# Kernel optimization log

Measured on AMD Instinct MI355X. Metric: run time of the kernel, lower is better.

The kernel has to match this reference:

```python
import jax, jax.numpy as jnp
import numpy as np

B, T, D, H = 2, 2048, 1024, 16
DH = D // H  # 64


def setup_inputs() -> dict:
    key = jax.random.key(0)
    ks = jax.random.split(key, 11)
    s = 1.0 / np.sqrt(D)
    return {
        "q": jax.random.normal(ks[0], (B, T, D), jnp.float32),
        "k": jax.random.normal(ks[1], (B, T, D), jnp.float32),
        "v": jax.random.normal(ks[2], (B, T, D), jnp.float32),
        "Wq": jax.random.normal(ks[3], (D, D), jnp.float32) * s,
        "bq": jnp.zeros((D,), jnp.float32),
        "Wk": jax.random.normal(ks[4], (D, D), jnp.float32) * s,
        "bk": jnp.zeros((D,), jnp.float32),
        "Wv": jax.random.normal(ks[5], (D, D), jnp.float32) * s,
        "bv": jnp.zeros((D,), jnp.float32),
        "Wo": jax.random.normal(ks[6], (D, D), jnp.float32) * s,
        "bo": jnp.zeros((D,), jnp.float32),
    }


def reference(q, k, v, Wq, bq, Wk, bk, Wv, bv, Wo, bo):
    Bq, Tq, _ = q.shape
    Tk = k.shape[1]
    # projections, split heads: [B, H, T, DH]
    qh = (q @ Wq + bq).reshape(Bq, Tq, H, DH).transpose(0, 2, 1, 3)
    kh = (k @ Wk + bk).reshape(Bq, Tk, H, DH).transpose(0, 2, 1, 3)
    vh = (v @ Wv + bv).reshape(Bq, Tk, H, DH).transpose(0, 2, 1, 3)
    # scores [B, H, Tq, Tk]
    scores = jnp.einsum("bhqd,bhkd->bhqk", qh, kh) / np.sqrt(DH)
    # causal mask with diagonal offset Tk - Tq (matches torch.tril semantics)
    ii = jnp.arange(Tq)[:, None]
    jj = jnp.arange(Tk)[None, :]
    causal = jj <= ii + (Tk - Tq)
    scores = jnp.where(causal, scores, -jnp.inf)
    attn = jax.nn.softmax(scores, axis=-1)
    x = jnp.einsum("bhqk,bhkd->bhqd", attn, vh)  # [B, H, Tq, DH]
    x = x.transpose(0, 2, 1, 3).reshape(Bq, Tq, H * DH)
    return x @ Wo + bo
```

## Files before the change

### kernel.cpp

```cpp
#include <hip/hip_runtime.h>

typedef unsigned short u16;
typedef unsigned int   u32;
typedef __attribute__((ext_vector_type(8)))  short short8;
typedef __attribute__((ext_vector_type(4)))  float f32x4;
typedef __attribute__((ext_vector_type(16))) float f32x16;
typedef __attribute__((ext_vector_type(2)))  u32 uint2v;
typedef __attribute__((ext_vector_type(4)))  u32 uint4v;

#define DEV __device__ __forceinline__

DEV u16 f2bf(float f) {
    u32 u = __builtin_bit_cast(u32, f);
    return (u16)((u + 0x7fffu + ((u >> 16) & 1u)) >> 16);
}
DEV float bf2f(u32 u) { return __builtin_bit_cast(float, u << 16); }
DEV u32 cvtpk(float a, float b) {
    u32 r;
    asm("v_cvt_pk_bf16_f32 %0, %1, %2" : "=v"(r) : "v"(a), "v"(b));
    return r;
}
typedef const __attribute__((address_space(1))) u32 g_u32;
typedef __attribute__((address_space(3))) u32 l_u32;
DEV void gload16(const u16* g, u16* l) {
    __builtin_amdgcn_global_load_lds((g_u32*)g, (l_u32*)l, 16, 0, 0);
}


template<int OMODE>
DEV void gemm_body(const u16* __restrict__ A_, const u16* __restrict__ Bt,
                   const float* __restrict__ bias, float oscale, void* C_) {
    constexpr int Kd = 1024;
    const int m0 = blockIdx.y * 128, n0 = blockIdx.x * 128;
    const int t = threadIdx.x, lane = t & 63, w = t >> 6;
    const int wm = w >> 1, wn = w & 1;
    const int l15 = lane & 15, l4 = lane >> 4;
    __shared__ __align__(16) u16 As[128 * 32];
    __shared__ __align__(16) u16 Bs[128 * 32];
    f32x4 acc[4][4] = {};

    for (int k0 = 0; k0 < Kd; k0 += 32) {
        #pragma unroll
        for (int rnd = 0; rnd < 2; rnd++) {
            int cc = rnd * 256 + t, row = cc >> 2, slot = cc & 3;
            gload16(Bt + (size_t)(n0 + row) * Kd + k0 + slot * 8, Bs + cc * 8);
            gload16(A_ + (size_t)(m0 + row) * Kd + k0 + slot * 8, As + cc * 8);
        }
        __syncthreads();
        short8 af[4], bfr[4];
        #pragma unroll
        for (int i = 0; i < 4; i++) {
            af[i]  = *(const short8*)(As + (wm * 64 + i * 16 + l15) * 32 + l4 * 8);
            bfr[i] = *(const short8*)(Bs + (wn * 64 + i * 16 + l15) * 32 + l4 * 8);
        }
        #pragma unroll
        for (int i = 0; i < 4; i++)
            #pragma unroll
            for (int j = 0; j < 4; j++)
                acc[i][j] = __builtin_amdgcn_mfma_f32_16x16x32_bf16(af[i], bfr[j], acc[i][j], 0, 0, 0);
        __syncthreads();
    }

    #pragma unroll
    for (int i = 0; i < 4; i++) {
        #pragma unroll
        for (int j = 0; j < 4; j++) {
            int col = n0 + wn * 64 + j * 16 + l15;
            int mb  = m0 + wm * 64 + i * 16 + l4 * 4;
            float bv = bias[col];
            if (OMODE == 2) {
                float* C = (float*)C_;
                #pragma unroll
                for (int r = 0; r < 4; r++)
                    C[(size_t)(mb + r) * 1024 + col] = acc[i][j][r] + bv;
            } else if (OMODE == 0) {
                u16* C = (u16*)C_;
                #pragma unroll
                for (int r = 0; r < 4; r++)
                    C[(size_t)(mb + r) * 1024 + col] = f2bf((acc[i][j][r] + bv) * oscale);
            } else if (OMODE == 3) {
                u16* C = (u16*)C_;
                int hh = col >> 6, dd = col & 63;
                int bb = mb >> 11, tt = mb & 2047;
                size_t tile = ((size_t)(bb * 16 + hh) * 64 + (tt >> 5)) * 2048;
                int c = dd >> 4, hi2 = (dd >> 3) & 1, e = dd & 7;
                int lob = tt & 31;
                #pragma unroll
                for (int r = 0; r < 4; r++)
                    C[tile + (size_t)((c * 2 + hi2) * 32 + lob + r) * 8 + e] =
                        f2bf(acc[i][j][r] + bv);
            } else {
                u16* C = (u16*)C_;
                int hh = col >> 6, dd = col & 63;
                int bb = mb >> 11, tt = mb & 2047;
                size_t tile = ((size_t)(bb * 16 + hh) * 64 + (tt >> 5)) * 2048;
                int tin = tt & 31, kc = tin >> 4, hi2 = (tin >> 3) & 1, e0 = tin & 7;
                int c2 = dd >> 5, lo2 = dd & 31;
                size_t off = tile + (size_t)((kc * 2 + c2) * 64 + hi2 * 32 + lo2) * 8 + e0;
                uint2v pp;
                pp[0] = cvtpk(acc[i][j][0] + bv, acc[i][j][1] + bv);
                pp[1] = cvtpk(acc[i][j][2] + bv, acc[i][j][3] + bv);
                *(uint2v*)(C + off) = pp;
            }
        }
    }
}

__global__ __launch_bounds__(256) void k_transw(const float* Wq, const float* Wk,
                                                const float* Wv, const float* Wo, u16* Wt) {
    int z = blockIdx.z;
    const float* W = z == 0 ? Wq : z == 1 ? Wk : z == 2 ? Wv : Wo;
    u16* O = Wt + (size_t)z * 1048576;
    __shared__ float tile[32][33];
    int n0 = blockIdx.x * 32, k0 = blockIdx.y * 32;
    int tx = threadIdx.x, ty = threadIdx.y;
    #pragma unroll
    for (int i = 0; i < 32; i += 8) tile[ty + i][tx] = W[(size_t)(k0 + ty + i) * 1024 + n0 + tx];
    __syncthreads();
    #pragma unroll
    for (int i = 0; i < 32; i += 8) O[(size_t)(n0 + ty + i) * 1024 + k0 + tx] = f2bf(tile[tx][ty + i]);
}

__global__ __launch_bounds__(256) void k_cvt(const float* q, const float* k, const float* v,
                                             u16* Abf) {
    int z = blockIdx.z;
    const float* src = z == 0 ? q : z == 1 ? k : v;
    u16* dst = Abf + (size_t)z * 4194304;
    size_t i = ((size_t)blockIdx.x * 256 + threadIdx.x) * 8;
    float4 a = *(const float4*)(src + i);
    float4 b = *(const float4*)(src + i + 4);
    uint4v o;
    o[0] = cvtpk(a.x, a.y); o[1] = cvtpk(a.z, a.w);
    o[2] = cvtpk(b.x, b.y); o[3] = cvtpk(b.z, b.w);
    *(uint4v*)(dst + i) = o;
}

__global__ __launch_bounds__(256) void k_proj(const u16* Abf, const u16* Wt,
                                              const float* bq, const float* bk,
                                              const float* bv, u16* QKV) {
    int z = blockIdx.z;
    if (z == 2)
        gemm_body<1>(Abf + (size_t)2 * 4194304, Wt + (size_t)2 * 1048576, bv, 1.f,
                     QKV + (size_t)2 * 4194304);
    else if (z == 1)
        gemm_body<3>(Abf + (size_t)4194304, Wt + (size_t)1048576, bk, 1.f,
                     QKV + (size_t)4194304);
    else
        gemm_body<0>(Abf, Wt, bq, 0.125f * 1.44269504088896f, QKV);
}

__global__ __launch_bounds__(256) void k_combine(const u16* Xp, const float* Lp, u16* Xc) {
    size_t idx = (size_t)blockIdx.x * 256 + threadIdx.x;
    size_t e = idx * 8;
    int row = (int)(e >> 10), hh = ((int)e & 1023) >> 6;
    float l0 = Lp[(size_t)row * 16 + hh];
    float l1 = Lp[65536 + (size_t)row * 16 + hh];
    float l2 = Lp[131072 + (size_t)row * 16 + hh];
    float s = 1.0f / (l0 + l1 + l2);
    float w0 = l0 * s, w1 = l1 * s, w2 = l2 * s;
    uint4v x0 = *(const uint4v*)(Xp + e);
    uint4v x1 = *(const uint4v*)(Xp + (size_t)4194304 + e);
    uint4v x2 = *(const uint4v*)(Xp + (size_t)2 * 4194304 + e);
    uint4v o;
    #pragma unroll
    for (int j = 0; j < 4; j++) {
        float a0 = bf2f(x0[j] & 0xffffu) * w0 + bf2f(x1[j] & 0xffffu) * w1
                 + bf2f(x2[j] & 0xffffu) * w2;
        float a1 = bf2f(x0[j] >> 16) * w0 + bf2f(x1[j] >> 16) * w1
                 + bf2f(x2[j] >> 16) * w2;
        o[j] = cvtpk(a0, a1);
    }
    *(uint4v*)(Xc + e) = o;
}

__global__ __launch_bounds__(256) void k_gemm_out(const u16* Xc, const u16* Wt,
                                                  const float* bo, float* out) {
    gemm_body<2>(Xc, Wt, bo, 1.f, out);
}

__global__ __launch_bounds__(256, 3) void k_attn(const u16* __restrict__ Qp,
                                                 const u16* __restrict__ Kp2,
                                                 const u16* __restrict__ Vp2,
                                                 u16* __restrict__ Xp, float* __restrict__ Lp) {
    const int id = (int)blockIdx.x;
    const int bh = id & 31;
    const int j = (id >> 5) & 15;
    const int par = id >> 9;
    const int b = bh >> 4, h = bh & 15;
    const int t = threadIdx.x, lane = t & 63, w = t >> 6;
    const int lo = lane & 31, hi = lane >> 5;
    const int qt = w * 16 + j;
    const int q0 = qt * 32;
    const int NTw = qt + 1;
    const u16* Qb = Qp + (size_t)(b * 2048) * 1024 + h * 64;
    const u16* Kb = Kp2 + (size_t)bh * 64 * 2048;
    const u16* Vb = Vp2 + (size_t)bh * 64 * 2048;

    short8 qf[4];
    #pragma unroll
    for (int c = 0; c < 4; c++)
        qf[c] = *(const short8*)(Qb + (size_t)(q0 + lo) * 1024 + c * 16 + hi * 8);

    f32x16 O0 = {}, O1 = {};
    float lsum = 0.f;
    const int qg = q0 + lo;

#define LOADKV(KF, VF, kt) do {                                                          \
        const u16* kt_ = Kb + (size_t)(kt) * 2048;                                       \
        const u16* vt_ = Vb + (size_t)(kt) * 2048;                                       \
        _Pragma("unroll")                                                                \
        for (int c = 0; c < 4; c++)                                                      \
            KF[c] = *(const short8*)(kt_ + c * 512 + lane * 8);                          \
        _Pragma("unroll")                                                                \
        for (int jj = 0; jj < 4; jj++)                                                   \
            VF[jj] = *(const short8*)(vt_ + jj * 512 + lane * 8);                        \
    } while (0)

#define COMPUTE(KF, VF, kt) do {                                                          \
        f32x16 S = {};                                                                    \
        _Pragma("unroll")                                                                 \
        for (int c = 0; c < 4; c++)                                                       \
            S = __builtin_amdgcn_mfma_f32_32x32x16_bf16(KF[c], qf[c], S, 0, 0, 0);        \
        const bool diag = ((kt) == NTw - 1);                                              \
        _Pragma("unroll")                                                                 \
        for (int kc = 0; kc < 2; kc++) {                                                  \
            float pv[8];                                                                  \
            _Pragma("unroll")                                                             \
            for (int jj = 0; jj < 8; jj++) {                                              \
                int r = kc * 8 + jj;                                                      \
                float s = S[r];                                                           \
                if (diag) {                                                               \
                    int kg = (kt) * 32 + (r & 3) + 8 * (r >> 2) + 4 * hi;                 \
                    s = (kg <= qg) ? s : -1e30f;                                          \
                }                                                                         \
                pv[jj] = __builtin_amdgcn_exp2f(s);                                       \
            }                                                                             \
            lsum += (((pv[0] + pv[1]) + (pv[2] + pv[3])) +                                \
                     ((pv[4] + pv[5]) + (pv[6] + pv[7])));                                \
            u32 w0 = cvtpk(pv[0], pv[1]), w1 = cvtpk(pv[2], pv[3]);                       \
            u32 w2 = cvtpk(pv[4], pv[5]), w3 = cvtpk(pv[6], pv[7]);                       \
            auto r0 = __builtin_amdgcn_permlane32_swap(w0, w2, false, false);             \
            auto r1 = __builtin_amdgcn_permlane32_swap(w1, w3, false, false);             \
            uint4v fw; fw[0] = r0[0]; fw[1] = r1[0]; fw[2] = r0[1]; fw[3] = r1[1];        \
            short8 pf = __builtin_bit_cast(short8, fw);                                   \
            O0 = __builtin_amdgcn_mfma_f32_32x32x16_bf16(pf, VF[kc * 2 + 0], O0, 0, 0, 0);\
            O1 = __builtin_amdgcn_mfma_f32_32x32x16_bf16(pf, VF[kc * 2 + 1], O1, 0, 0, 0);\
        }                                                                                 \
    } while (0)

    {
        short8 kf0[4], vf0[4], kf1[4], vf1[4];
        int kt = par;
        if (kt < NTw) {
            LOADKV(kf0, vf0, kt);
            while (true) {
                if (kt + 3 < NTw) LOADKV(kf1, vf1, kt + 3);
                COMPUTE(kf0, vf0, kt);
                kt += 3;
                if (kt >= NTw) break;
                if (kt + 3 < NTw) LOADKV(kf0, vf0, kt + 3);
                COMPUTE(kf1, vf1, kt);
                kt += 3;
                if (kt >= NTw) break;
            }
        }
    }
#undef LOADKV
#undef COMPUTE

    float ltot = lsum + __shfl_xor(lsum, 32, 64);
    u16* Xb = Xp + (size_t)par * 4194304;
    #pragma unroll
    for (int r = 0; r < 16; r++) {
        int qr = (r & 3) + 8 * (r >> 2) + 4 * hi;
        float lt = __shfl(ltot, qr, 64);
        float linv = lt > 0.f ? 1.f / lt : 0.f;
        size_t rowb = (size_t)(b * 2048 + q0 + qr) * 1024 + h * 64;
        Xb[rowb + lo]      = f2bf(O0[r] * linv);
        Xb[rowb + 32 + lo] = f2bf(O1[r] * linv);
    }
    if (hi == 0)
        Lp[(size_t)par * 65536 + (size_t)(b * 2048 + q0 + lo) * 16 + h] = ltot;
}

extern "C" void kernel_launch(void* const* d_in, const int* in_sizes, int n_in,
                              void* d_out, int out_size, void* d_ws, size_t ws_size,
                              hipStream_t stream) {
    (void)in_sizes; (void)n_in; (void)out_size; (void)ws_size;
    const float* q  = (const float*)d_in[0];
    const float* k  = (const float*)d_in[1];
    const float* v  = (const float*)d_in[2];
    const float* Wq = (const float*)d_in[3];
    const float* bq = (const float*)d_in[4];
    const float* Wk = (const float*)d_in[5];
    const float* bk = (const float*)d_in[6];
    const float* Wv = (const float*)d_in[7];
    const float* bv = (const float*)d_in[8];
    const float* Wo = (const float*)d_in[9];
    const float* bo = (const float*)d_in[10];

    u16*   Wt  = (u16*)d_ws;
    u16*   QKV = Wt + (size_t)4 * 1048576;
    u16*   Abf = QKV + (size_t)3 * 4194304;
    u16*   Xp  = Abf;
    u16*   Xc  = QKV;
    float* Lp  = (float*)(Abf + (size_t)3 * 4194304);

    k_transw<<<dim3(32, 32, 4), dim3(32, 8), 0, stream>>>(Wq, Wk, Wv, Wo, Wt);
    k_cvt<<<dim3(2048, 1, 3), 256, 0, stream>>>(q, k, v, Abf);
    k_proj<<<dim3(8, 32, 3), 256, 0, stream>>>(Abf, Wt, bq, bk, bv, QKV);
    k_attn<<<dim3(1536), 256, 0, stream>>>(QKV, QKV + (size_t)4194304,
                                           QKV + (size_t)2 * 4194304, Xp, Lp);
    k_combine<<<2048, 256, 0, stream>>>(Xp, Lp, Xc);
    k_gemm_out<<<dim3(8, 32), 256, 0, stream>>>(Xc, Wt + (size_t)3 * 1048576,
                                                bo, (float*)d_out);
}
```

Baseline: 126.7 us.

## Pre-pack GEMM operands into MFMA fragment order for contiguous loads

The producer kernels (weight transpose, input convert, combine) now write bf16 operands in a tiled 16x32 fragment-packed layout, so each GEMM k-step loads one contiguous 1KB chunk per 16-row tile. LDS reads become lane-linear and avoid the strided row pattern with its possible bank conflicts. The GEMM template is also turned into a runtime omode branch, which may add branching and register pressure in the epilogue. Producer stores are now scattered, which can reduce their write coalescing.

Result: slower. 135.1 us (+6.6%).

```diff
diff --git a/kernel.cpp b/kernel.cpp
--- a/kernel.cpp
+++ b/kernel.cpp
@@ -27,10 +27,9 @@
 }
 
 
-template<int OMODE>
-DEV void gemm_body(const u16* __restrict__ A_, const u16* __restrict__ Bt,
-                   const float* __restrict__ bias, float oscale, void* C_) {
-    constexpr int Kd = 1024;
+DEV void gemm_body(const u16* __restrict__ Apk, const u16* __restrict__ Bpk,
+                   const float* __restrict__ bias, float oscale, void* C_,
+                   int omode) {
     const int m0 = blockIdx.y * 128, n0 = blockIdx.x * 128;
     const int t = threadIdx.x, lane = t & 63, w = t >> 6;
     const int wm = w >> 1, wn = w & 1;
@@ -39,19 +38,21 @@
     __shared__ __align__(16) u16 Bs[128 * 32];
     f32x4 acc[4][4] = {};
 
-    for (int k0 = 0; k0 < Kd; k0 += 32) {
+    const int rtA = m0 >> 4, rtB = n0 >> 4;
+    for (int k0 = 0; k0 < 1024; k0 += 32) {
+        const int ct = k0 >> 5;
         #pragma unroll
         for (int rnd = 0; rnd < 2; rnd++) {
-            int cc = rnd * 256 + t, row = cc >> 2, slot = cc & 3;
-            gload16(Bt + (size_t)(n0 + row) * Kd + k0 + slot * 8, Bs + cc * 8);
-            gload16(A_ + (size_t)(m0 + row) * Kd + k0 + slot * 8, As + cc * 8);
+            int cc = rnd * 256 + t, s = cc >> 6, l = cc & 63;
+            gload16(Bpk + (size_t)(((rtB + s) * 32 + ct) * 64 + l) * 8, Bs + cc * 8);
+            gload16(Apk + (size_t)(((rtA + s) * 32 + ct) * 64 + l) * 8, As + cc * 8);
         }
         __syncthreads();
         short8 af[4], bfr[4];
         #pragma unroll
         for (int i = 0; i < 4; i++) {
-            af[i]  = *(const short8*)(As + (wm * 64 + i * 16 + l15) * 32 + l4 * 8);
-            bfr[i] = *(const short8*)(Bs + (wn * 64 + i * 16 + l15) * 32 + l4 * 8);
+            af[i]  = *(const short8*)(As + ((wm * 4 + i) * 64 + lane) * 8);
+            bfr[i] = *(const short8*)(Bs + ((wn * 4 + i) * 64 + lane) * 8);
         }
         #pragma unroll
         for (int i = 0; i < 4; i++)
@@ -68,17 +69,17 @@
             int col = n0 + wn * 64 + j * 16 + l15;
             int mb  = m0 + wm * 64 + i * 16 + l4 * 4;
             float bv = bias[col];
-            if (OMODE == 2) {
+            if (omode == 2) {
                 float* C = (float*)C_;
                 #pragma unroll
                 for (int r = 0; r < 4; r++)
                     C[(size_t)(mb + r) * 1024 + col] = acc[i][j][r] + bv;
-            } else if (OMODE == 0) {
+            } else if (omode == 0) {
                 u16* C = (u16*)C_;
                 #pragma unroll
                 for (int r = 0; r < 4; r++)
                     C[(size_t)(mb + r) * 1024 + col] = f2bf((acc[i][j][r] + bv) * oscale);
-            } else if (OMODE == 3) {
+            } else if (omode == 3) {
                 u16* C = (u16*)C_;
                 int hh = col >> 6, dd = col & 63;
                 int bb = mb >> 11, tt = mb & 2047;
@@ -118,7 +119,12 @@
     for (int i = 0; i < 32; i += 8) tile[ty + i][tx] = W[(size_t)(k0 + ty + i) * 1024 + n0 + tx];
     __syncthreads();
     #pragma unroll
-    for (int i = 0; i < 32; i += 8) O[(size_t)(n0 + ty + i) * 1024 + k0 + tx] = f2bf(tile[tx][ty + i]);
+    for (int i = 0; i < 32; i += 8) {
+        int n = n0 + ty + i, k = k0 + tx;
+        size_t pi = ((size_t)((n >> 4) * 32 + (k >> 5)) * 64
+                     + ((n & 15) + 16 * ((k >> 3) & 3))) * 8 + (k & 7);
+        O[pi] = f2bf(tile[tx][ty + i]);
+    }
 }
 
 __global__ __launch_bounds__(256) void k_cvt(const float* q, const float* k, const float* v,
@@ -127,32 +133,34 @@
     const float* src = z == 0 ? q : z == 1 ? k : v;
     u16* dst = Abf + (size_t)z * 4194304;
     size_t i = ((size_t)blockIdx.x * 256 + threadIdx.x) * 8;
+    int row = (int)(i >> 10), col = (int)i & 1023;
     float4 a = *(const float4*)(src + i);
     float4 b = *(const float4*)(src + i + 4);
     uint4v o;
     o[0] = cvtpk(a.x, a.y); o[1] = cvtpk(a.z, a.w);
     o[2] = cvtpk(b.x, b.y); o[3] = cvtpk(b.z, b.w);
-    *(uint4v*)(dst + i) = o;
+    size_t pi = ((size_t)((row >> 4) * 32 + (col >> 5)) * 64
+                 + ((row & 15) + 16 * ((col >> 3) & 3))) * 8;
+    *(uint4v*)(dst + pi) = o;
 }
 
 __global__ __launch_bounds__(256) void k_proj(const u16* Abf, const u16* Wt,
                                               const float* bq, const float* bk,
                                               const float* bv, u16* QKV) {
     int z = blockIdx.z;
-    if (z == 2)
-        gemm_body<1>(Abf + (size_t)2 * 4194304, Wt + (size_t)2 * 1048576, bv, 1.f,
-                     QKV + (size_t)2 * 4194304);
-    else if (z == 1)
-        gemm_body<3>(Abf + (size_t)4194304, Wt + (size_t)1048576, bk, 1.f,
-                     QKV + (size_t)4194304);
-    else
-        gemm_body<0>(Abf, Wt, bq, 0.125f * 1.44269504088896f, QKV);
+    const u16* A_ = Abf + (size_t)z * 4194304;
+    const u16* B_ = Wt + (size_t)z * 1048576;
+    const float* bias = z == 0 ? bq : z == 1 ? bk : bv;
+    int omode = z == 0 ? 0 : (z == 1 ? 3 : 1);
+    float oscale = z == 0 ? 0.125f * 1.44269504088896f : 1.f;
+    void* C_ = QKV + (size_t)z * 4194304;
+    gemm_body(A_, B_, bias, oscale, C_, omode);
 }
 
 __global__ __launch_bounds__(256) void k_combine(const u16* Xp, const float* Lp, u16* Xc) {
     size_t idx = (size_t)blockIdx.x * 256 + threadIdx.x;
     size_t e = idx * 8;
-    int row = (int)(e >> 10), hh = ((int)e & 1023) >> 6;
+    int row = (int)(e >> 10), col = (int)e & 1023, hh = col >> 6;
     float l0 = Lp[(size_t)row * 16 + hh];
     float l1 = Lp[65536 + (size_t)row * 16 + hh];
     float l2 = Lp[131072 + (size_t)row * 16 + hh];
@@ -170,12 +178,14 @@
                  + bf2f(x2[j] >> 16) * w2;
         o[j] = cvtpk(a0, a1);
     }
-    *(uint4v*)(Xc + e) = o;
+    size_t pi = ((size_t)((row >> 4) * 32 + (col >> 5)) * 64
+                 + ((row & 15) + 16 * ((col >> 3) & 3))) * 8;
+    *(uint4v*)(Xc + pi) = o;
 }
 
 __global__ __launch_bounds__(256) void k_gemm_out(const u16* Xc, const u16* Wt,
                                                   const float* bo, float* out) {
-    gemm_body<2>(Xc, Wt, bo, 1.f, out);
+    gemm_body(Xc, Wt, bo, 1.f, out, 2);
 }
 
 __global__ __launch_bounds__(256, 3) void k_attn(const u16* __restrict__ Qp,
```
